# Kernel optimization log

Measured on AMD Instinct MI355X. Metric: run time of the kernel, lower is better.

## Reference

```python
import jax, jax.numpy as jnp
import numpy as np

B, P, D, H, L = 1024, 22, 3, 64, 4
HS = P + 1  # 22-dim one-hot atom type + 1 time channel
N = B * P


def _edges():
    # fully-connected directed edges (no self loops) per graph, batched with node offsets
    idx = np.arange(P)
    r, c = np.meshgrid(idx, idx, indexing='ij')
    m = r != c
    r0, c0 = r[m], c[m]
    off = (P * np.arange(B))[:, None]
    row = (r0[None, :] + off).reshape(-1)
    col = (c0[None, :] + off).reshape(-1)
    return row.astype(np.int32), col.astype(np.int32)


def setup_inputs() -> dict:
    key = jax.random.key(0)
    ks = jax.random.split(key, 12)
    s = 0.02
    row, col = _edges()
    return dict(
        input_array=jax.random.normal(ks[0], (B, P * D), jnp.float32),
        time_array=jax.random.uniform(ks[1], (B,), jnp.float32),
        emb_w=jax.random.normal(ks[2], (HS, H), jnp.float32) * s,
        emb_b=jnp.zeros((H,), jnp.float32),
        edge_w1=jax.random.normal(ks[3], (L, 2 * H + 2, H), jnp.float32) * s,
        edge_b1=jnp.zeros((L, H), jnp.float32),
        edge_w2=jax.random.normal(ks[4], (L, H, H), jnp.float32) * s,
        edge_b2=jnp.zeros((L, H), jnp.float32),
        node_w1=jax.random.normal(ks[5], (L, 2 * H, H), jnp.float32) * s,
        node_b1=jnp.zeros((L, H), jnp.float32),
        node_w2=jax.random.normal(ks[6], (L, H, H), jnp.float32) * s,
        node_b2=jnp.zeros((L, H), jnp.float32),
        cm_w1=jax.random.normal(ks[7], (L, H, H), jnp.float32) * s,
        cm_b1=jnp.zeros((L, H), jnp.float32),
        cm_w2=jax.random.normal(ks[8], (L, H, 1), jnp.float32) * 0.001,  # xavier gain=0.001 final layer
        cc_w1=jax.random.normal(ks[9], (L, H, H), jnp.float32) * s,
        cc_b1=jnp.zeros((L, H), jnp.float32),
        cc_w2=jax.random.normal(ks[10], (L, H, 1), jnp.float32) * 0.001,
        row=jnp.asarray(row),
        col=jnp.asarray(col),
    )


def reference(input_array, time_array, emb_w, emb_b, edge_w1, edge_b1, edge_w2, edge_b2,
              node_w1, node_b1, node_w2, node_b2, cm_w1, cm_b1, cm_w2,
              cc_w1, cc_b1, cc_w2, row, col):
    silu = jax.nn.silu
    x0 = input_array.reshape(N, D)
    # h_initial: one-hot atom types repeated over batch, plus time channel
    h = jnp.tile(jnp.eye(P, dtype=input_array.dtype), (B, 1))  # [N, 22]
    t = jnp.repeat(time_array[:, None], P, axis=1).reshape(N, 1)
    h = jnp.concatenate([h, t], axis=1)  # [N, 23]
    # edge_attr = squared distance at initial coords (fixed across layers)
    edge_attr = jnp.sum((x0[row] - x0[col]) ** 2, axis=1, keepdims=True)  # [E,1]
    h = h @ emb_w + emb_b  # embedding
    x = x0
    seg = lambda d: jax.ops.segment_sum(d, row, num_segments=N)
    for l in range(L):
        diff = x[row] - x[col]                                   # [E,3]
        radial = jnp.sum(diff ** 2, axis=1, keepdims=True)       # [E,1]
        coord_diff = diff / (jnp.sqrt(radial + 1e-8) + 1)
        e_in = jnp.concatenate([h[row], h[col], radial, edge_attr], axis=1)
        ef = silu(silu(e_in @ edge_w1[l] + edge_b1[l]) @ edge_w2[l] + edge_b2[l])  # [E,H]
        cross = jnp.cross(x[row], x[col])                        # [E,3]
        cross = cross / (jnp.sqrt(jnp.sum(cross ** 2, axis=1, keepdims=True) + 1e-8) + 1)
        cm = silu(ef @ cm_w1[l] + cm_b1[l]) @ cm_w2[l]           # [E,1]
        cc = silu(ef @ cc_w1[l] + cc_b1[l]) @ cc_w2[l]           # [E,1]
        trans = coord_diff * cm + cc * cross                     # [E,3]
        x = x + seg(trans)                                       # agg='sum'
        agg = jnp.concatenate([h, seg(ef)], axis=1)              # [N,2H]
        h = h + (silu(agg @ node_w1[l] + node_b1[l]) @ node_w2[l] + node_b2[l])  # recurrent
    vel = (x - x0).reshape(B, P, D)
    vel = vel - jnp.mean(vel, axis=1, keepdims=True)  # remove_mean
    return vel.reshape(B, P * D)
```

## Files before the change

### kernel.cpp

```cpp
#include <hip/hip_runtime.h>
#include <hip/hip_bf16.h>
#include <math.h>

#define PP 22
#define HH 64
#define NL 4
#define NE 462
#define NTILE 29
#define SST 68

typedef __attribute__((ext_vector_type(8))) short bf16x8;
typedef __attribute__((ext_vector_type(4))) float f32x4;

#define MFMA(A, B, C) __builtin_amdgcn_mfma_f32_16x16x32_bf16(A, B, C, 0, 0, 0)
#define PHI(mt, r) ((((mt) >> 1) << 5) + (((r) >> 2) << 3) + (((mt) & 1) << 2) + ((r) & 3))

__device__ __forceinline__ float silu_f(float v) { return v / (1.0f + __expf(-v)); }

__device__ __forceinline__ unsigned short f2bf(float x) {
    __hip_bfloat16 h = __float2bfloat16(x);
    unsigned short u;
    __builtin_memcpy(&u, &h, 2);
    return u;
}

#define LD8(dst, PTR) { \
    float4 _a = *(const float4*)(PTR); float4 _b = *(const float4*)((PTR) + 4); \
    dst[0]=_a.x; dst[1]=_a.y; dst[2]=_a.z; dst[3]=_a.w; \
    dst[4]=_b.x; dst[5]=_b.y; dst[6]=_b.z; dst[7]=_b.w; }

__global__ __launch_bounds__(64) void prep_w(
    const float* __restrict__ edge_w1, const float* __restrict__ edge_w2,
    const float* __restrict__ cm_w1, const float* __restrict__ cc_w1,
    const float* __restrict__ node_w1, const float* __restrict__ node_w2,
    unsigned short* __restrict__ ws)
{
    int blk = blockIdx.x;
    int l = blk >> 6, moff = blk & 63;
    int lane = threadIdx.x, n0 = lane & 15, kg = lane >> 4;
    const float* base; int col, kt;
    if (moff < 8)       { kt = moff >> 2;              int nt = moff & 3;        base = edge_w1 + l * 130 * HH;           col = nt * 16 + n0; }
    else if (moff < 16) { int m = moff - 8;  kt = m >> 2; int nt = m & 3;        base = edge_w1 + l * 130 * HH + 64 * HH; col = nt * 16 + n0; }
    else if (moff < 24) { int m = moff - 16; kt = m >> 2; int mt = m & 3;        base = edge_w2 + l * HH * HH;            col = PHI(mt, n0); }
    else if (moff < 32) { int m = moff - 24; kt = m >> 2; int nt = m & 3;        base = cm_w1 + l * HH * HH;              col = nt * 16 + n0; }
    else if (moff < 40) { int m = moff - 32; kt = m >> 2; int nt = m & 3;        base = cc_w1 + l * HH * HH;              col = nt * 16 + n0; }
    else if (moff < 56) { int m = moff - 40; kt = m >> 2; int mt = m & 3;        base = node_w1 + l * 128 * HH;           col = PHI(mt, n0); }
    else                { int m = moff - 56; kt = m >> 2; int nt = m & 3;        base = node_w2 + l * HH * HH;            col = nt * 16 + n0; }
    int k0 = kt * 32 + kg * 8;
    unsigned short* d = ws + blk * 512 + lane * 8;
#pragma unroll
    for (int j = 0; j < 8; ++j) d[j] = f2bf(base[(k0 + j) * HH + col]);
}

__global__ __launch_bounds__(256, 3) void egnn_kernel(
    const float* __restrict__ input, const float* __restrict__ timev,
    const float* __restrict__ emb_w, const float* __restrict__ emb_b,
    const float* __restrict__ edge_w1, const float* __restrict__ edge_b1,
    const float* __restrict__ edge_b2,
    const float* __restrict__ node_b1, const float* __restrict__ node_b2,
    const float* __restrict__ cm_b1, const float* __restrict__ cm_w2,
    const float* __restrict__ cc_b1, const float* __restrict__ cc_w2,
    const unsigned short* __restrict__ wfr,
    float* __restrict__ out)
{
    const int g    = blockIdx.x;
    const int tid  = threadIdx.x;
    const int w    = tid >> 6;
    const int lane = tid & 63;
    const int n0   = lane & 15;
    const int kg   = lane >> 4;

    __shared__ float sApre[PP][SST], sBpre[PP][SST];
    __shared__ float sh[PP][SST], sSeg[PP][SST];
    __shared__ float scd[NE][3], scr[NE][3];
    __shared__ __align__(16) float sx[PP][4];
    __shared__ __align__(16) float sx0[PP][4];
    __shared__ float sTr[PP][4];
    __shared__ float sW128[HH], sW129[HH];
    __shared__ float sBp[128];
    __shared__ float sHC[256];
    __shared__ float smean[3];

    if (tid < PP * 3) {
        float v = input[g * (PP * 3) + tid];
        sx0[tid / 3][tid % 3] = v;
        sx [tid / 3][tid % 3] = v;
    }
    if (tid < PP) { sx0[tid][3] = 0.f; sx[tid][3] = 0.f; }
    {
        float tg = timev[g];
        for (int i = w; i < PP; i += 4)
            sh[i][lane] = emb_w[i * HH + lane] + tg * emb_w[PP * HH + lane] + emb_b[lane];
    }
    for (int idx = tid; idx < PP * SST; idx += 256) (&sSeg[0][0])[idx] = 0.f;
    if (tid < PP * 4) (&sTr[0][0])[tid] = 0.f;
    __syncthreads();

    for (int l = 0; l < NL; ++l) {
        const unsigned short* wfl = wfr + (size_t)l * 32768;

        for (int e = tid; e < NE; e += 256) {
            int a = e % PP, r = e / PP;
            int b = (r < a) ? r : r + 1;
            float4 xa = *(const float4*)&sx[a][0];
            float4 xb = *(const float4*)&sx[b][0];
            float dx = xa.x - xb.x, dy = xa.y - xb.y, dz = xa.z - xb.z;
            float rad = dx * dx + dy * dy + dz * dz;
            float inv = 1.0f / (sqrtf(rad + 1e-8f) + 1.0f);
            scd[e][0] = dx * inv; scd[e][1] = dy * inv; scd[e][2] = dz * inv;
            float cx = xa.y * xb.z - xa.z * xb.y;
            float cy = xa.z * xb.x - xa.x * xb.z;
            float cz = xa.x * xb.y - xa.y * xb.x;
            float cn = 1.0f / (sqrtf(cx * cx + cy * cy + cz * cz + 1e-8f) + 1.0f);
            scr[e][0] = cx * cn; scr[e][1] = cy * cn; scr[e][2] = cz * cn;
        }
        if (tid < HH)          sW128[tid]      = edge_w1[(l * 130 + 128) * HH + tid];
        else if (tid < 2 * HH) sW129[tid - HH] = edge_w1[(l * 130 + 129) * HH + tid - HH];
        if (tid < 128) {
            int i = tid & 63, mt = i >> 4, r = i & 15;
            int phi = PHI(mt, r);
            sBp[tid] = (tid < 64) ? edge_b2[l * HH + phi] : node_b1[l * HH + phi];
        }
        {
            int i = tid & 63, arr = tid >> 6;
            const float* src = (arr == 0) ? cm_b1 : (arr == 1) ? cc_b1 : (arr == 2) ? cm_w2 : cc_w2;
            sHC[tid] = src[l * HH + i];
        }
        {
            int mtn = w & 1, mat = w >> 1;
            int node = mtn * 16 + n0;
            bool vn = node < PP;
            int crow = vn ? node : 0;
            bf16x8 hhi[2];
#pragma unroll
            for (int kt = 0; kt < 2; ++kt) {
                float vv[8];
                LD8(vv, &sh[crow][kt * 32 + kg * 8]);
#pragma unroll
                for (int j = 0; j < 8; ++j)
                    hhi[kt][j] = (short)f2bf(vn ? vv[j] : 0.f);
            }
#pragma unroll 2
            for (int ntf = 0; ntf < 4; ++ntf) {
                f32x4 acc = (f32x4){0.f, 0.f, 0.f, 0.f};
#pragma unroll
                for (int kt = 0; kt < 2; ++kt) {
                    bf16x8 wv = *(const bf16x8*)(wfl + (mat * 8 + kt * 4 + ntf) * 512 + lane * 8);
                    acc = MFMA(hhi[kt], wv, acc);
                }
                int col = ntf * 16 + n0;
                float b1v = edge_b1[l * HH + col];
#pragma unroll
                for (int q = 0; q < 4; ++q) {
                    int m = mtn * 16 + kg * 4 + q;
                    if (m < PP) {
                        if (mat == 0) sApre[m][col] = acc[q] + b1v;
                        else          sBpre[m][col] = acc[q];
                    }
                }
            }
        }
        __syncthreads();

        bf16x8 wE2[2][4], wCM[2][4], wCC[2][4];
#pragma unroll
        for (int kt = 0; kt < 2; ++kt)
#pragma unroll
            for (int mt = 0; mt < 4; ++mt) {
                wE2[kt][mt] = *(const bf16x8*)(wfl + (16 + kt * 4 + mt) * 512 + lane * 8);
                wCM[kt][mt] = *(const bf16x8*)(wfl + (24 + kt * 4 + mt) * 512 + lane * 8);
                wCC[kt][mt] = *(const bf16x8*)(wfl + (32 + kt * 4 + mt) * 512 + lane * 8);
            }

        for (int jt = w; jt < NTILE; jt += 4) {
            int e0 = jt * 16;
            int e = e0 + n0;
            bool vr = e < NE;
            int ec = vr ? e : (NE - 1);
            int a = ec % PP, r = ec / PP;
            int b = (r < a) ? r : r + 1;
            float4 xa = *(const float4*)&sx[a][0];
            float4 xb = *(const float4*)&sx[b][0];
            float4 oa = *(const float4*)&sx0[a][0];
            float4 ob = *(const float4*)&sx0[b][0];
            float dx = xa.x - xb.x, dy = xa.y - xb.y, dz = xa.z - xb.z;
            float rad = dx * dx + dy * dy + dz * dz;
            float ex = oa.x - ob.x, ey = oa.y - ob.y, ez = oa.z - ob.z;
            float ea = ex * ex + ey * ey + ez * ez;

            f32x4 acc[4];
#pragma unroll
            for (int mt = 0; mt < 4; ++mt) acc[mt] = (f32x4){0.f, 0.f, 0.f, 0.f};
#pragma unroll
            for (int kt = 0; kt < 2; ++kt) {
                int base = kt * 32 + kg * 8;
                float av[8], bv[8], w8[8], w9[8];
                LD8(av, &sApre[a][base]);
                LD8(bv, &sBpre[b][base]);
                LD8(w8, &sW128[base]);
                LD8(w9, &sW129[base]);
                bf16x8 zhi;
#pragma unroll
                for (int j8 = 0; j8 < 8; ++j8) {
                    float z = av[j8] + bv[j8] + rad * w8[j8] + ea * w9[j8];
                    zhi[j8] = (short)f2bf(silu_f(z));
                }
#pragma unroll
                for (int mt = 0; mt < 4; ++mt)
                    acc[mt] = MFMA(wE2[kt][mt], zhi, acc[mt]);
            }
            unsigned short pk[4][4];
#pragma unroll
            for (int mt = 0; mt < 4; ++mt) {
                int phib = ((mt >> 1) << 5) + (kg << 3) + ((mt & 1) << 2);
#pragma unroll
                for (int q = 0; q < 4; ++q) {
                    float v = silu_f(acc[mt][q] + sBp[mt * 16 + kg * 4 + q]);
                    v = vr ? v : 0.f;
                    pk[mt][q] = f2bf(v);
                    if (vr) atomicAdd(&sSeg[a][phib + q], v);
                }
            }
            bf16x8 ehi[2];
#pragma unroll
            for (int kt = 0; kt < 2; ++kt)
#pragma unroll
                for (int j8 = 0; j8 < 8; ++j8)
                    ehi[kt][j8] = (short)pk[kt * 2 + (j8 >> 2)][j8 & 3];

            float pm[4] = {0.f, 0.f, 0.f, 0.f}, pc[4] = {0.f, 0.f, 0.f, 0.f};
#pragma unroll
            for (int nt = 0; nt < 4; ++nt) {
                f32x4 am = (f32x4){0.f, 0.f, 0.f, 0.f};
                f32x4 ac = (f32x4){0.f, 0.f, 0.f, 0.f};
#pragma unroll
                for (int kt = 0; kt < 2; ++kt) {
                    am = MFMA(ehi[kt], wCM[kt][nt], am);
                    ac = MFMA(ehi[kt], wCC[kt][nt], ac);
                }
                float cmb = sHC[nt * 16 + n0];
                float ccb = sHC[64 + nt * 16 + n0];
                float cm2 = sHC[128 + nt * 16 + n0];
                float cc2 = sHC[192 + nt * 16 + n0];
#pragma unroll
                for (int q = 0; q < 4; ++q) {
                    pm[q] += silu_f(am[q] + cmb) * cm2;
                    pc[q] += silu_f(ac[q] + ccb) * cc2;
                }
            }
#pragma unroll
            for (int q = 0; q < 4; ++q) {
#pragma unroll
                for (int off = 1; off <= 8; off <<= 1) {
                    pm[q] += __shfl_xor(pm[q], off);
                    pc[q] += __shfl_xor(pc[q], off);
                }
            }
            if (n0 < 3) {
#pragma unroll
                for (int q = 0; q < 4; ++q) {
                    int gE = e0 + kg * 4 + q;
                    if (gE < NE) {
                        int a2 = gE % PP;
                        atomicAdd(&sTr[a2][n0], scd[gE][n0] * pm[q] + pc[q] * scr[gE][n0]);
                    }
                }
            }
        }
        __syncthreads();

        unsigned short pk[4][4];
        {
            int mtn = w >> 1;
            int node = mtn * 16 + n0;
            bool vn = node < PP;
            int crow = vn ? node : 0;
            f32x4 acc[4];
#pragma unroll
            for (int mt = 0; mt < 4; ++mt) acc[mt] = (f32x4){0.f, 0.f, 0.f, 0.f};
#pragma unroll 2
            for (int kt = 0; kt < 4; ++kt) {
                const float* srcp = (kt < 2) ? &sh[crow][kt * 32 + kg * 8]
                                             : &sSeg[crow][(kt - 2) * 32 + kg * 8];
                float vv[8];
                LD8(vv, srcp);
                bf16x8 bhi;
#pragma unroll
                for (int j8 = 0; j8 < 8; ++j8)
                    bhi[j8] = (short)f2bf(vn ? vv[j8] : 0.f);
#pragma unroll
                for (int mt = 0; mt < 4; ++mt) {
                    bf16x8 wv = *(const bf16x8*)(wfl + (40 + kt * 4 + mt) * 512 + lane * 8);
                    acc[mt] = MFMA(wv, bhi, acc[mt]);
                }
            }
#pragma unroll
            for (int mt = 0; mt < 4; ++mt)
#pragma unroll
                for (int q = 0; q < 4; ++q)
                    pk[mt][q] = f2bf(silu_f(acc[mt][q] + sBp[64 + mt * 16 + kg * 4 + q]));
        }
        __syncthreads();

        {
            bf16x8 mh[2];
#pragma unroll
            for (int kt = 0; kt < 2; ++kt)
#pragma unroll
                for (int j8 = 0; j8 < 8; ++j8)
                    mh[kt][j8] = (short)pk[kt * 2 + (j8 >> 2)][j8 & 3];
            int mtn = w >> 1;
#pragma unroll
            for (int t = 0; t < 2; ++t) {
                int ntf = (w & 1) * 2 + t;
                f32x4 acc = (f32x4){0.f, 0.f, 0.f, 0.f};
#pragma unroll
                for (int kt = 0; kt < 2; ++kt) {
                    bf16x8 wv = *(const bf16x8*)(wfl + (56 + kt * 4 + ntf) * 512 + lane * 8);
                    acc = MFMA(mh[kt], wv, acc);
                }
                int col = ntf * 16 + n0;
                float nb2 = node_b2[l * HH + col];
#pragma unroll
                for (int q = 0; q < 4; ++q) {
                    int m = mtn * 16 + kg * 4 + q;
                    if (m < PP) sh[m][col] += acc[q] + nb2;
                }
            }
        }
        if (tid < PP * 4) {
            int p = tid >> 2, d = tid & 3;
            float v = sTr[p][d];
            if (d < 3) sx[p][d] += v;
            sTr[p][d] = 0.f;
        }
        for (int idx = tid; idx < PP * SST; idx += 256) (&sSeg[0][0])[idx] = 0.f;
        __syncthreads();
    }

    if (tid < 3) {
        float s = 0.0f;
        for (int p = 0; p < PP; ++p) s += sx[p][tid] - sx0[p][tid];
        smean[tid] = s / (float)PP;
    }
    __syncthreads();
    if (tid < PP * 3) {
        int p = tid / 3, d = tid % 3;
        out[g * (PP * 3) + tid] = (sx[p][d] - sx0[p][d]) - smean[d];
    }
}

extern "C" void kernel_launch(void* const* d_in, const int* in_sizes, int n_in,
                              void* d_out, int out_size, void* d_ws, size_t ws_size,
                              hipStream_t stream) {
    const float* input   = (const float*)d_in[0];
    const float* timev   = (const float*)d_in[1];
    const float* emb_w   = (const float*)d_in[2];
    const float* emb_b   = (const float*)d_in[3];
    const float* edge_w1 = (const float*)d_in[4];
    const float* edge_b1 = (const float*)d_in[5];
    const float* edge_w2 = (const float*)d_in[6];
    const float* edge_b2 = (const float*)d_in[7];
    const float* node_w1 = (const float*)d_in[8];
    const float* node_b1 = (const float*)d_in[9];
    const float* node_w2 = (const float*)d_in[10];
    const float* node_b2 = (const float*)d_in[11];
    const float* cm_w1   = (const float*)d_in[12];
    const float* cm_b1   = (const float*)d_in[13];
    const float* cm_w2   = (const float*)d_in[14];
    const float* cc_w1   = (const float*)d_in[15];
    const float* cc_b1   = (const float*)d_in[16];
    const float* cc_w2   = (const float*)d_in[17];

    unsigned short* wsu = (unsigned short*)d_ws;
    prep_w<<<dim3(NL * 64), dim3(64), 0, stream>>>(edge_w1, edge_w2, cm_w1, cc_w1,
                                                   node_w1, node_w2, wsu);

    float* out = (float*)d_out;
    egnn_kernel<<<dim3(1024), dim3(256), 0, stream>>>(
        input, timev, emb_w, emb_b, edge_w1, edge_b1, edge_b2,
        node_b1, node_b2, cm_b1, cm_w2, cc_b1, cc_w2, wsu, out);
}
```

Measured before the change: 881.3 us.

## Stage per-layer weights in LDS, fuse geometry into edge tiles, swap CM/CC MFMA operands

```diff
diff --git a/kernel.cpp b/kernel.cpp
--- a/kernel.cpp
+++ b/kernel.cpp
@@ -22,6 +22,9 @@
     unsigned short u;
     __builtin_memcpy(&u, &h, 2);
     return u;
+}
+__device__ __forceinline__ float bfbits(unsigned int u, int hi) {
+    return __uint_as_float(((u >> (hi * 16)) & 0xffffu) << 16);
 }
 
 #define LD8(dst, PTR) { \
@@ -70,16 +73,19 @@
     const int n0   = lane & 15;
     const int kg   = lane >> 4;
 
+    __shared__ __align__(16) unsigned short wlds[12288];
     __shared__ float sApre[PP][SST], sBpre[PP][SST];
     __shared__ float sh[PP][SST], sSeg[PP][SST];
-    __shared__ float scd[NE][3], scr[NE][3];
     __shared__ __align__(16) float sx[PP][4];
     __shared__ __align__(16) float sx0[PP][4];
     __shared__ float sTr[PP][4];
     __shared__ float sW128[HH], sW129[HH];
     __shared__ float sBp[128];
-    __shared__ float sHC[256];
+    __shared__ unsigned int sHCp[4][32];
     __shared__ float smean[3];
+
+#define STAGE(SRC, N16) { const uint4* _s = (const uint4*)(SRC); uint4* _d = (uint4*)wlds; \
+    for (int idx = tid; idx < (N16); idx += 256) _d[idx] = _s[idx]; }
 
     if (tid < PP * 3) {
         float v = input[g * (PP * 3) + tid];
@@ -99,33 +105,24 @@
     for (int l = 0; l < NL; ++l) {
         const unsigned short* wfl = wfr + (size_t)l * 32768;
 
-        for (int e = tid; e < NE; e += 256) {
-            int a = e % PP, r = e / PP;
-            int b = (r < a) ? r : r + 1;
-            float4 xa = *(const float4*)&sx[a][0];
-            float4 xb = *(const float4*)&sx[b][0];
-            float dx = xa.x - xb.x, dy = xa.y - xb.y, dz = xa.z - xb.z;
-            float rad = dx * dx + dy * dy + dz * dz;
-            float inv = 1.0f / (sqrtf(rad + 1e-8f) + 1.0f);
-            scd[e][0] = dx * inv; scd[e][1] = dy * inv; scd[e][2] = dz * inv;
-            float cx = xa.y * xb.z - xa.z * xb.y;
-            float cy = xa.z * xb.x - xa.x * xb.z;
-            float cz = xa.x * xb.y - xa.y * xb.x;
-            float cn = 1.0f / (sqrtf(cx * cx + cy * cy + cz * cz + 1e-8f) + 1.0f);
-            scr[e][0] = cx * cn; scr[e][1] = cy * cn; scr[e][2] = cz * cn;
-        }
-        if (tid < HH)          sW128[tid]      = edge_w1[(l * 130 + 128) * HH + tid];
-        else if (tid < 2 * HH) sW129[tid - HH] = edge_w1[(l * 130 + 129) * HH + tid - HH];
-        if (tid < 128) {
-            int i = tid & 63, mt = i >> 4, r = i & 15;
+        STAGE(wfl, 1024);
+        if (tid < HH)               sW128[tid]        = edge_w1[(l * 130 + 128) * HH + tid];
+        else if (tid < 2 * HH)      sW129[tid - HH]   = edge_w1[(l * 130 + 129) * HH + tid - HH];
+        else {
+            int t2 = tid - 2 * HH;
+            int i = t2 & 63, mt = i >> 4, r = i & 15;
             int phi = PHI(mt, r);
-            sBp[tid] = (tid < 64) ? edge_b2[l * HH + phi] : node_b1[l * HH + phi];
-        }
-        {
-            int i = tid & 63, arr = tid >> 6;
+            sBp[t2] = (t2 < 64) ? edge_b2[l * HH + phi] : node_b1[l * HH + phi];
+        }
+        if (tid >= 128) {
+            int t3 = tid - 128;
+            int arr = t3 >> 5, j = t3 & 31;
             const float* src = (arr == 0) ? cm_b1 : (arr == 1) ? cc_b1 : (arr == 2) ? cm_w2 : cc_w2;
-            sHC[tid] = src[l * HH + i];
-        }
+            sHCp[arr][j] = (unsigned)f2bf(src[l * HH + 2 * j])
+                         | ((unsigned)f2bf(src[l * HH + 2 * j + 1]) << 16);
+        }
+        __syncthreads();
+
         {
             int mtn = w & 1, mat = w >> 1;
             int node = mtn * 16 + n0;
@@ -140,12 +137,12 @@
                 for (int j = 0; j < 8; ++j)
                     hhi[kt][j] = (short)f2bf(vn ? vv[j] : 0.f);
             }
-#pragma unroll 2
+#pragma unroll
             for (int ntf = 0; ntf < 4; ++ntf) {
                 f32x4 acc = (f32x4){0.f, 0.f, 0.f, 0.f};
 #pragma unroll
                 for (int kt = 0; kt < 2; ++kt) {
-                    bf16x8 wv = *(const bf16x8*)(wfl + (mat * 8 + kt * 4 + ntf) * 512 + lane * 8);
+                    bf16x8 wv = *(const bf16x8*)&wlds[(mat * 8 + kt * 4 + ntf) * 512 + lane * 8];
                     acc = MFMA(hhi[kt], wv, acc);
                 }
                 int col = ntf * 16 + n0;
@@ -162,14 +159,25 @@
         }
         __syncthreads();
 
-        bf16x8 wE2[2][4], wCM[2][4], wCC[2][4];
+        STAGE(wfl + 16 * 512, 1536);
+        __syncthreads();
+
+        bf16x8 wE2r[2][4], wCMr[2][4], wCCr[2][4];
 #pragma unroll
         for (int kt = 0; kt < 2; ++kt)
 #pragma unroll
             for (int mt = 0; mt < 4; ++mt) {
-                wE2[kt][mt] = *(const bf16x8*)(wfl + (16 + kt * 4 + mt) * 512 + lane * 8);
-                wCM[kt][mt] = *(const bf16x8*)(wfl + (24 + kt * 4 + mt) * 512 + lane * 8);
-                wCC[kt][mt] = *(const bf16x8*)(wfl + (32 + kt * 4 + mt) * 512 + lane * 8);
+                wE2r[kt][mt] = *(const bf16x8*)&wlds[(kt * 4 + mt) * 512 + lane * 8];
+                wCMr[kt][mt] = *(const bf16x8*)&wlds[(8 + kt * 4 + mt) * 512 + lane * 8];
+                wCCr[kt][mt] = *(const bf16x8*)&wlds[(16 + kt * 4 + mt) * 512 + lane * 8];
+            }
+        unsigned int bP[4][4][2];
+#pragma unroll
+        for (int arr = 0; arr < 4; ++arr)
+#pragma unroll
+            for (int nt = 0; nt < 4; ++nt) {
+                bP[arr][nt][0] = sHCp[arr][nt * 8 + kg * 2];
+                bP[arr][nt][1] = sHCp[arr][nt * 8 + kg * 2 + 1];
             }
 
         for (int jt = w; jt < NTILE; jt += 4) {
@@ -187,6 +195,13 @@
             float rad = dx * dx + dy * dy + dz * dz;
             float ex = oa.x - ob.x, ey = oa.y - ob.y, ez = oa.z - ob.z;
             float ea = ex * ex + ey * ey + ez * ez;
+            float inv = 1.0f / (sqrtf(rad + 1e-8f) + 1.0f);
+            float cdx = dx * inv, cdy = dy * inv, cdz = dz * inv;
+            float cx = xa.y * xb.z - xa.z * xb.y;
+            float cy = xa.z * xb.x - xa.x * xb.z;
+            float cz = xa.x * xb.y - xa.y * xb.x;
+            float cn = 1.0f / (sqrtf(cx * cx + cy * cy + cz * cz + 1e-8f) + 1.0f);
+            float crx = cx * cn, cry = cy * cn, crz = cz * cn;
 
             f32x4 acc[4];
 #pragma unroll
@@ -207,9 +222,9 @@
                 }
 #pragma unroll
                 for (int mt = 0; mt < 4; ++mt)
-                    acc[mt] = MFMA(wE2[kt][mt], zhi, acc[mt]);
-            }
-            unsigned short pk[4][4];
+                    acc[mt] = MFMA(wE2r[kt][mt], zhi, acc[mt]);
+            }
+            unsigned short pkE[4][4];
 #pragma unroll
             for (int mt = 0; mt < 4; ++mt) {
                 int phib = ((mt >> 1) << 5) + (kg << 3) + ((mt & 1) << 2);
@@ -217,7 +232,7 @@
                 for (int q = 0; q < 4; ++q) {
                     float v = silu_f(acc[mt][q] + sBp[mt * 16 + kg * 4 + q]);
                     v = vr ? v : 0.f;
-                    pk[mt][q] = f2bf(v);
+                    pkE[mt][q] = f2bf(v);
                     if (vr) atomicAdd(&sSeg[a][phib + q], v);
                 }
             }
@@ -226,50 +241,46 @@
             for (int kt = 0; kt < 2; ++kt)
 #pragma unroll
                 for (int j8 = 0; j8 < 8; ++j8)
-                    ehi[kt][j8] = (short)pk[kt * 2 + (j8 >> 2)][j8 & 3];
-
-            float pm[4] = {0.f, 0.f, 0.f, 0.f}, pc[4] = {0.f, 0.f, 0.f, 0.f};
+                    ehi[kt][j8] = (short)pkE[kt * 2 + (j8 >> 2)][j8 & 3];
+
+            float pm = 0.f, pc = 0.f;
 #pragma unroll
             for (int nt = 0; nt < 4; ++nt) {
                 f32x4 am = (f32x4){0.f, 0.f, 0.f, 0.f};
                 f32x4 ac = (f32x4){0.f, 0.f, 0.f, 0.f};
 #pragma unroll
                 for (int kt = 0; kt < 2; ++kt) {
-                    am = MFMA(ehi[kt], wCM[kt][nt], am);
-                    ac = MFMA(ehi[kt], wCC[kt][nt], ac);
-                }
-                float cmb = sHC[nt * 16 + n0];
-                float ccb = sHC[64 + nt * 16 + n0];
-                float cm2 = sHC[128 + nt * 16 + n0];
-                float cc2 = sHC[192 + nt * 16 + n0];
+                    am = MFMA(wCMr[kt][nt], ehi[kt], am);
+                    ac = MFMA(wCCr[kt][nt], ehi[kt], ac);
+                }
 #pragma unroll
                 for (int q = 0; q < 4; ++q) {
-                    pm[q] += silu_f(am[q] + cmb) * cm2;
-                    pc[q] += silu_f(ac[q] + ccb) * cc2;
-                }
-            }
-#pragma unroll
-            for (int q = 0; q < 4; ++q) {
-#pragma unroll
-                for (int off = 1; off <= 8; off <<= 1) {
-                    pm[q] += __shfl_xor(pm[q], off);
-                    pc[q] += __shfl_xor(pc[q], off);
-                }
-            }
-            if (n0 < 3) {
-#pragma unroll
-                for (int q = 0; q < 4; ++q) {
-                    int gE = e0 + kg * 4 + q;
-                    if (gE < NE) {
-                        int a2 = gE % PP;
-                        atomicAdd(&sTr[a2][n0], scd[gE][n0] * pm[q] + pc[q] * scr[gE][n0]);
-                    }
-                }
-            }
-        }
-        __syncthreads();
-
-        unsigned short pk[4][4];
+                    int hi = q & 1, pj = q >> 1;
+                    float cmb = bfbits(bP[0][nt][pj], hi);
+                    float ccb = bfbits(bP[1][nt][pj], hi);
+                    float cm2 = bfbits(bP[2][nt][pj], hi);
+                    float cc2 = bfbits(bP[3][nt][pj], hi);
+                    pm += silu_f(am[q] + cmb) * cm2;
+                    pc += silu_f(ac[q] + ccb) * cc2;
+                }
+            }
+            pm += __shfl_xor(pm, 16, 64);
+            pm += __shfl_xor(pm, 32, 64);
+            pc += __shfl_xor(pc, 16, 64);
+            pc += __shfl_xor(pc, 32, 64);
+            if (kg == 0 && vr) {
+                atomicAdd(&sTr[a][0], cdx * pm + pc * crx);
+                atomicAdd(&sTr[a][1], cdy * pm + pc * cry);
+                atomicAdd(&sTr[a][2], cdz * pm + pc * crz);
+            }
+            __builtin_amdgcn_sched_barrier(0);
+        }
+        __syncthreads();
+
+        STAGE(wfl + 40 * 512, 1536);
+        __syncthreads();
+
+        unsigned short pkN[4][4];
         {
             int mtn = w >> 1;
             int node = mtn * 16 + n0;
@@ -278,7 +289,7 @@
             f32x4 acc[4];
 #pragma unroll
             for (int mt = 0; mt < 4; ++mt) acc[mt] = (f32x4){0.f, 0.f, 0.f, 0.f};
-#pragma unroll 2
+#pragma unroll
             for (int kt = 0; kt < 4; ++kt) {
                 const float* srcp = (kt < 2) ? &sh[crow][kt * 32 + kg * 8]
                                              : &sSeg[crow][(kt - 2) * 32 + kg * 8];
@@ -290,7 +301,7 @@
                     bhi[j8] = (short)f2bf(vn ? vv[j8] : 0.f);
 #pragma unroll
                 for (int mt = 0; mt < 4; ++mt) {
-                    bf16x8 wv = *(const bf16x8*)(wfl + (40 + kt * 4 + mt) * 512 + lane * 8);
+                    bf16x8 wv = *(const bf16x8*)&wlds[(kt * 4 + mt) * 512 + lane * 8];
                     acc[mt] = MFMA(wv, bhi, acc[mt]);
                 }
             }
@@ -298,7 +309,7 @@
             for (int mt = 0; mt < 4; ++mt)
 #pragma unroll
                 for (int q = 0; q < 4; ++q)
-                    pk[mt][q] = f2bf(silu_f(acc[mt][q] + sBp[64 + mt * 16 + kg * 4 + q]));
+                    pkN[mt][q] = f2bf(silu_f(acc[mt][q] + sBp[64 + mt * 16 + kg * 4 + q]));
         }
         __syncthreads();
 
@@ -308,7 +319,7 @@
             for (int kt = 0; kt < 2; ++kt)
 #pragma unroll
                 for (int j8 = 0; j8 < 8; ++j8)
-                    mh[kt][j8] = (short)pk[kt * 2 + (j8 >> 2)][j8 & 3];
+                    mh[kt][j8] = (short)pkN[kt * 2 + (j8 >> 2)][j8 & 3];
             int mtn = w >> 1;
 #pragma unroll
             for (int t = 0; t < 2; ++t) {
@@ -316,7 +327,7 @@
                 f32x4 acc = (f32x4){0.f, 0.f, 0.f, 0.f};
 #pragma unroll
                 for (int kt = 0; kt < 2; ++kt) {
-                    bf16x8 wv = *(const bf16x8*)(wfl + (56 + kt * 4 + ntf) * 512 + lane * 8);
+                    bf16x8 wv = *(const bf16x8*)&wlds[(16 + kt * 4 + ntf) * 512 + lane * 8];
                     acc = MFMA(mh[kt], wv, acc);
                 }
                 int col = ntf * 16 + n0;
@@ -348,6 +359,7 @@
         int p = tid / 3, d = tid % 3;
         out[g * (PP * 3) + tid] = (sx[p][d] - sx0[p][d]) - smean[d];
     }
+#undef STAGE
 }
 
 extern "C" void kernel_launch(void* const* d_in, const int* in_sizes, int n_in,
```

After: 1.026 ms. +16.4%, slower.
